# Performance work log

Hardware: AMD Instinct MI355X
Metric: run time of the kernel (lower is better)

## Reference

```python
import jax, jax.numpy as jnp
import numpy as np
from jax import lax

B = 4096          # number of utterance nodes
D_IN = 1856       # 512 audio + 512 visual + 768 text + 64 speaker
H = 128           # hidden_dim
N_STEPS = 4       # fixed-step RK4 steps over t in [0, 1]
ALPHA1, ALPHA2, BETA = 0.8, 0.5, 0.1


def setup_inputs() -> dict:
    key = jax.random.key(0)
    ks = jax.random.split(key, 10)
    features = jax.random.normal(ks[0], (B, D_IN), dtype=jnp.float32)
    speaker_ids = jax.random.randint(ks[1], (B,), 0, 12)
    modality_masks = jax.random.uniform(ks[2], (B, 3), dtype=jnp.float32)
    # params stored as [in, out]; y = x @ W + b (matches torch Linear math)
    s_in = 1.0 / np.sqrt(D_IN)
    Wp = jax.random.uniform(ks[3], (D_IN, H), minval=-s_in, maxval=s_in, dtype=jnp.float32)
    bp = jax.random.uniform(ks[4], (H,), minval=-s_in, maxval=s_in, dtype=jnp.float32)
    s1 = 1.0 / np.sqrt(2 * H)
    W1 = jax.random.uniform(ks[5], (2 * H, H), minval=-s1, maxval=s1, dtype=jnp.float32)
    b1 = jax.random.uniform(ks[6], (H,), minval=-s1, maxval=s1, dtype=jnp.float32)
    s2 = 1.0 / np.sqrt(H)
    W2 = jax.random.uniform(ks[7], (H, H), minval=-s2, maxval=s2, dtype=jnp.float32)
    b2 = jax.random.uniform(ks[8], (H,), minval=-s2, maxval=s2, dtype=jnp.float32)
    return {"features": features, "speaker_ids": speaker_ids,
            "modality_masks": modality_masks, "Wp": Wp, "bp": bp,
            "W1": W1, "b1": b1, "W2": W2, "b2": b2}


def build_graph(speaker_ids, modality_masks):
    idx = jnp.arange(B)
    time_diff = jnp.abs(idx[:, None] - idx[None, :]).astype(jnp.float32)  # [B,B]
    temporal = jnp.exp(-BETA * time_diff)
    same_spk = speaker_ids[:, None] == speaker_ids[None, :]
    # mean_c |m_i,c - m_j,c| without materializing [B,B,3]
    mod_diff = sum(jnp.abs(modality_masks[:, c][:, None] - modality_masks[:, c][None, :])
                   for c in range(3)) * (1.0 / 3.0)
    mod_sim = 1.0 - mod_diff
    off_diag = jnp.where(same_spk, ALPHA1 * temporal, ALPHA2 * temporal * mod_sim)
    adj = jnp.where(idx[:, None] == idx[None, :], 1.0, off_diag)
    adj = adj / (adj.sum(axis=-1, keepdims=True) + 1e-8)
    return adj


def reference(features, speaker_ids, modality_masks, Wp, bp, W1, b1, W2, b2):
    h0 = features @ Wp + bp                      # [B,H] input projection
    adj = build_graph(speaker_ids, modality_masks)

    def ode_func(h):
        h_neighbors = adj @ h                    # [B,H] neighbor aggregation
        h_combined = jnp.concatenate([h, h_neighbors], axis=-1)  # [B,2H]
        return jnp.tanh(h_combined @ W1 + b1) @ W2 + b2

    dt = 1.0 / N_STEPS

    def rk4_step(h, _):
        k1 = ode_func(h)
        k2 = ode_func(h + 0.5 * dt * k1)
        k3 = ode_func(h + 0.5 * dt * k2)
        k4 = ode_func(h + dt * k3)
        return h + (dt / 6.0) * (k1 + 2.0 * k2 + 2.0 * k3 + k4), None

    h_final, _ = lax.scan(rk4_step, h0, None, length=N_STEPS)
    return h_final
```

## Files before the change

kernel.cpp:

```cpp
#include <hip/hip_runtime.h>


typedef unsigned short u16;
typedef unsigned long long u64;
typedef __attribute__((ext_vector_type(8))) short bf16x8v;
typedef __attribute__((ext_vector_type(4))) float f32x4;

#define MFMA16(a, b, c) __builtin_amdgcn_mfma_f32_16x16x32_bf16(a, b, c, 0, 0, 0)

#define BN 4096
#define HN 128
#define DIN 1856
#define TILEW 320

__device__ __forceinline__ float bf2f(u16 u) {
  union { unsigned u; float f; } v; v.u = ((unsigned)u) << 16; return v.f;
}
__device__ __forceinline__ u16 f2bf(float f) {
  union { float f; unsigned u; } v; v.f = f;
  unsigned u = v.u;
  return (u16)((u + 0x7fffu + ((u >> 16) & 1u)) >> 16);
}
__device__ __forceinline__ float ldx(const void* p, long idx, int isf) {
  return isf ? ((const float*)p)[idx] : bf2f(((const u16*)p)[idx]);
}

__device__ __forceinline__ void cstore8(u16* p, u64 v) {
  __hip_atomic_store((u64*)p, v, __ATOMIC_RELAXED, __HIP_MEMORY_SCOPE_AGENT);
}

__global__ __launch_bounds__(256) void detect(
    const void* a0, const void* a1, const void* a2, const void* a3,
    const void* a4, const void* a5, const void* a6, const void* a7,
    const unsigned* spk_raw, int* flags) {
  __shared__ int part[256];
  const int b = blockIdx.x, t = threadIdx.x;
  int cnt = 0;
  if (b < 8) {
    const void* arr[8] = {a0, a1, a2, a3, a4, a5, a6, a7};
    const int nel[8] = {BN * DIN, BN * 3, DIN * HN, HN, 2 * HN * HN, HN, HN * HN, HN};
    const u16* p = (const u16*)arr[b];
    int ns = nel[b] / 2; if (ns > 512) ns = 512;
    for (int e = t; e < ns; e += 256) {
      unsigned ex = (p[2 * e] >> 7) & 0xFFu;
      if (ex < 64u) cnt++;
    }
  } else {
    for (int e = t; e < 512; e += 256)
      if (spk_raw[2 * e + 1] != 0u) cnt++;
  }
  part[t] = cnt;
  __syncthreads();
  #pragma unroll
  for (int o = 128; o > 0; o >>= 1) {
    if (t < o) part[t] += part[t + o];
    __syncthreads();
  }
  if (t == 0) {
    if (b < 8) flags[b] = (part[0] >= 2) ? 1 : 0;
    else       flags[9] = (part[0] == 0) ? 1 : 0;
  }
}

#define FEATBLK 3712
__global__ __launch_bounds__(256) void prep(
    const void* feat, const void* Wp, const void* W1, const void* W2,
    const void* masks, const void* spk, const int* __restrict__ flags,
    u16* featc, u16* WpT, u16* W1T, u16* W2T, float* masks_c, int* spk_c) {
  const int blk = blockIdx.x, t = threadIdx.x;
  if (blk < FEATBLK) {
    long e = ((long)blk * 256 + t) * 8;
    if (flags[0]) {
      const float* pf = (const float*)feat + e;
      u16 r[8];
      #pragma unroll
      for (int k = 0; k < 8; k++) r[k] = f2bf(pf[k]);
      *(bf16x8v*)(featc + e) = *(bf16x8v*)r;
    } else {
      *(bf16x8v*)(featc + e) = *(const bf16x8v*)((const u16*)feat + e);
    }
    return;
  }
  long e = (long)(blk - FEATBLK) * 256 + t;
  const int nWp = DIN * HN, nW1 = 2 * HN * HN, nW2 = HN * HN, nM = BN * 3;
  if (e < nWp) {
    int k = e >> 7, o = e & 127;
    WpT[(long)o * DIN + k] = f2bf(ldx(Wp, e, flags[2]));
    return;
  }
  e -= nWp;
  if (e < nW1) { int k = e >> 7, o = e & 127; W1T[(long)o * 256 + k] = f2bf(ldx(W1, e, flags[4])); return; }
  e -= nW1;
  if (e < nW2) { int k = e >> 7, o = e & 127; W2T[(long)o * 128 + k] = f2bf(ldx(W2, e, flags[6])); return; }
  e -= nW2;
  if (e < nM) { masks_c[e] = ldx(masks, e, flags[1]); return; }
  e -= nM;
  if (e < BN) spk_c[e] = flags[9] ? ((const int*)spk)[2 * e] : ((const int*)spk)[e];
}

__global__ __launch_bounds__(256) void prep2(
    const void* x0, const void* x1, const void* x2,
    const int* __restrict__ flags, float* bp_c, float* b1c, float* b2c) {
  __shared__ float mxs[3][64];
  __shared__ int ord[3];
  const void* bs[3] = {x0, x1, x2};
  const int fl[3] = {flags[3], flags[5], flags[7]};
  const int t = threadIdx.x;
  if (t < 192) {
    int a = t / 64, e = t % 64;
    mxs[a][e] = fmaxf(fabsf(ldx(bs[a], e, fl[a])), fabsf(ldx(bs[a], e + 64, fl[a])));
  }
  __syncthreads();
  if (t == 0) {
    float mx[3];
    for (int a = 0; a < 3; a++) {
      float m = 0.f;
      for (int e = 0; e < 64; e++) m = fmaxf(m, mxs[a][e]);
      mx[a] = m;
    }
    int imin = 0, imax = 0;
    for (int k = 1; k < 3; k++) { if (mx[k] < mx[imin]) imin = k; if (mx[k] > mx[imax]) imax = k; }
    int imid = 3 - imin - imax;
    if (imin == imax) { imin = 0; imid = 1; imax = 2; }
    ord[0] = imin; ord[1] = imid; ord[2] = imax;
  }
  __syncthreads();
  if (t < HN) {
    bp_c[t] = ldx(bs[ord[0]], t, fl[ord[0]]);
    b1c[t]  = ldx(bs[ord[1]], t, fl[ord[1]]);
    b2c[t]  = ldx(bs[ord[2]], t, fl[ord[2]]);
  }
}

__device__ __forceinline__ float adj_raw(int i, int j, int si, float m0, float m1, float m2,
                                         const int* __restrict__ spk,
                                         const float* __restrict__ mk) {
  if (i == j) return 1.0f;
  float t = expf(-0.1f * fabsf((float)(i - j)));
  if (spk[j] == si) return 0.8f * t;
  float ms = fabsf(m0 - mk[j * 3]) + fabsf(m1 - mk[j * 3 + 1]) + fabsf(m2 - mk[j * 3 + 2]);
  return 0.5f * t * (1.0f - ms * (1.0f / 3.0f));
}

__global__ __launch_bounds__(256) void build_band(
    const int* __restrict__ spk, const float* __restrict__ mk, u16* __restrict__ band,
    int* __restrict__ syncf) {
  __shared__ float part[256];
  __shared__ float invs;
  const int i = blockIdx.x, t = threadIdx.x;
  if (t == 0 && i < 256) syncf[i] = 0;
  const int si = spk[i];
  const float m0 = mk[i * 3], m1 = mk[i * 3 + 1], m2 = mk[i * 3 + 2];
  float s = 0.f;
  for (int j = t; j < BN; j += 256) s += adj_raw(i, j, si, m0, m1, m2, spk, mk);
  part[t] = s;
  __syncthreads();
  if (t == 0) {
    float tot = 0.f;
    for (int k = 0; k < 256; k++) tot += part[k];
    invs = 1.0f / (tot + 1e-8f);
  }
  __syncthreads();
  const float inv = invs;
  const int jbase = (i & ~15) - 128;
  for (int k = t; k < TILEW; k += 256) {
    int j = jbase + k;
    float v = 0.f;
    if (j >= 0 && j < BN) v = adj_raw(i, j, si, m0, m1, m2, spk, mk) * inv;
    band[(long)i * TILEW + k] = f2bf(v);
  }
}

#define SNAP_ELEMS ((size_t)HN * BN + 8192)

__global__ __launch_bounds__(512, 2) void fused_ode(
    const u16* __restrict__ featc, const u16* __restrict__ WpT,
    const float* __restrict__ bp_c, const u16* __restrict__ band,
    const u16* __restrict__ W1T, const u16* __restrict__ W2T,
    const float* __restrict__ b1c, const float* __restrict__ b2c,
    u16* __restrict__ hsb, float* __restrict__ outp,
    int* __restrict__ syncf) {
  __shared__ u16 hc[16][264];
  __shared__ u16 zt[16][136];

  const int tid = threadIdx.x, w = tid >> 6, lane = tid & 63;
  const int m = lane & 15, q = lane >> 4;
  const int blk = blockIdx.x;
  const int tile = ((blk & 7) << 5) | (blk >> 3);
  const int r0 = tile * 16, jb = r0 - 128;
  const int n0 = w * 16 + m;
  const int i0 = r0 + q * 4;
  const long base = (long)n0 * BN + i0;

  int nbr = tile - 8 + tid;
  nbr = nbr < 0 ? 0 : (nbr > 255 ? 255 : nbr);

  bf16x8v w1r[8], w2r[4], bnd[10];
  {
    const u16* w1row = W1T + (long)n0 * 256;
    #pragma unroll
    for (int kf = 0; kf < 8; kf++) {
      int k = (kf >> 1) * 64 + (kf & 1) * 32 + q * 8;
      w1r[kf] = *(const bf16x8v*)(w1row + k);
    }
    const u16* w2row = W2T + (long)n0 * 128;
    #pragma unroll
    for (int kf = 0; kf < 4; kf++) {
      int k = (kf >> 1) * 64 + (kf & 1) * 32 + q * 8;
      w2r[kf] = *(const bf16x8v*)(w2row + k);
    }
    const u16* bandrow = band + (long)tile * 5120 + m * TILEW;
    #pragma unroll
    for (int kf = 0; kf < 10; kf++) {
      int k = (kf >> 1) * 64 + (kf & 1) * 32 + q * 8;
      bnd[kf] = *(const bf16x8v*)(bandrow + k);
    }
  }
  const float b1v = b1c[n0], b2v = b2c[n0];

  f32x4 hb;
  {
    f32x4 a0 = {0, 0, 0, 0};
    const u16* arow = featc + (long)(r0 + m) * DIN;
    const u16* brow = WpT + (long)n0 * DIN;
    #pragma unroll 4
    for (int kf = 0; kf < 58; kf++) {
      int k = (kf >> 1) * 64 + (kf & 1) * 32 + q * 8;
      bf16x8v a = *(const bf16x8v*)(arow + k);
      bf16x8v b = *(const bf16x8v*)(brow + k);
      a0 = MFMA16(a, b, a0);
    }
    a0 += bp_c[n0];
    hb = a0;
  }
  f32x4 acc = {0, 0, 0, 0};
  {
    u16* snap0 = hsb + 4096;
    ushort4 hsv;
    hsv.x = f2bf(hb[0]); hsv.y = f2bf(hb[1]); hsv.z = f2bf(hb[2]); hsv.w = f2bf(hb[3]);
    union { ushort4 s; u64 q8; } pu; pu.s = hsv;
    cstore8(&snap0[base], pu.q8);
    hc[q * 4 + 0][n0] = hsv.x; hc[q * 4 + 1][n0] = hsv.y;
    hc[q * 4 + 2][n0] = hsv.z; hc[q * 4 + 3][n0] = hsv.w;
  }
  asm volatile("s_waitcnt vmcnt(0)" ::: "memory");
  __syncthreads();
  if (tid == 0)
    __hip_atomic_store(&syncf[tile], 1, __ATOMIC_RELAXED, __HIP_MEMORY_SCOPE_AGENT);

  const float dt6 = 0.25f / 6.0f;

  #pragma unroll 1
  for (int s = 0; s < 16; s++) {
    const int sub = s & 3;

    if (tid < 20) {
      while (__hip_atomic_load(&syncf[nbr], __ATOMIC_RELAXED,
                               __HIP_MEMORY_SCOPE_AGENT) < s + 1)
        __builtin_amdgcn_s_sleep(1);
    }
    __syncthreads();

    f32x4 g0 = {0, 0, 0, 0};
    const u16* hrow = hsb + (size_t)s * SNAP_ELEMS + 4096 + (long)n0 * BN + jb;
    #pragma unroll
    for (int kf = 0; kf < 10; kf++) {
      int k = (kf >> 1) * 64 + (kf & 1) * 32 + q * 8;
      bf16x8v b = *(const bf16x8v*)(hrow + k);
      g0 = MFMA16(bnd[kf], b, g0);
    }
    #pragma unroll
    for (int r = 0; r < 4; r++) hc[q * 4 + r][128 + n0] = f2bf(g0[r]);
    __syncthreads();

    f32x4 z0 = {0, 0, 0, 0};
    #pragma unroll
    for (int kf = 0; kf < 8; kf++) {
      int k = (kf >> 1) * 64 + (kf & 1) * 32 + q * 8;
      bf16x8v a = *(const bf16x8v*)&hc[m][k];
      z0 = MFMA16(a, w1r[kf], z0);
    }
    #pragma unroll
    for (int r = 0; r < 4; r++) zt[q * 4 + r][n0] = f2bf(tanhf(z0[r] + b1v));
    __syncthreads();

    f32x4 k0 = {0, 0, 0, 0};
    #pragma unroll
    for (int kf = 0; kf < 4; kf++) {
      int k = (kf >> 1) * 64 + (kf & 1) * 32 + q * 8;
      bf16x8v a = *(const bf16x8v*)&zt[m][k];
      k0 = MFMA16(a, w2r[kf], k0);
    }
    f32x4 kv = k0;
    kv += b2v;

    f32x4 hn;
    if (sub == 0)      { acc = 1.f * kv;  hn = hb + 0.125f * kv; }
    else if (sub == 1) { acc += 2.f * kv; hn = hb + 0.125f * kv; }
    else if (sub == 2) { acc += 2.f * kv; hn = hb + 0.25f  * kv; }
    else {
      hn = hb + dt6 * (acc + kv);
      hb = hn;
      if (s == 15) {
        #pragma unroll
        for (int r = 0; r < 4; r++) outp[(long)(i0 + r) * HN + n0] = hn[r];
      }
    }

    if (s < 15) {
      u16* snapw = hsb + (size_t)(s + 1) * SNAP_ELEMS + 4096;
      ushort4 hsv;
      hsv.x = f2bf(hn[0]); hsv.y = f2bf(hn[1]); hsv.z = f2bf(hn[2]); hsv.w = f2bf(hn[3]);
      union { ushort4 s4; u64 q8; } pu; pu.s4 = hsv;
      cstore8(&snapw[base], pu.q8);
      hc[q * 4 + 0][n0] = hsv.x; hc[q * 4 + 1][n0] = hsv.y;
      hc[q * 4 + 2][n0] = hsv.z; hc[q * 4 + 3][n0] = hsv.w;
      asm volatile("s_waitcnt vmcnt(0)" ::: "memory");
      __syncthreads();
      if (tid == 0)
        __hip_atomic_store(&syncf[tile], s + 2, __ATOMIC_RELAXED, __HIP_MEMORY_SCOPE_AGENT);
    }
  }
}

extern "C" void kernel_launch(void* const* d_in, const int* in_sizes, int n_in,
                              void* d_out, int out_size, void* d_ws, size_t ws_size,
                              hipStream_t stream) {
  const void* feat = nullptr; const void* spk = nullptr; const void* masks = nullptr;
  const void* Wp = nullptr; const void* W1 = nullptr; const void* W2 = nullptr;
  const void* bias[3] = {nullptr, nullptr, nullptr};
  int nb = 0;
  for (int k = 0; k < n_in; k++) {
    switch (in_sizes[k]) {
      case BN * DIN:    feat = d_in[k]; break;
      case BN:          spk = d_in[k]; break;
      case BN * 3:      masks = d_in[k]; break;
      case DIN * HN:    Wp = d_in[k]; break;
      case 2 * HN * HN: W1 = d_in[k]; break;
      case HN * HN:     W2 = d_in[k]; break;
      default:          if (in_sizes[k] == HN && nb < 3) bias[nb++] = d_in[k]; break;
    }
  }
  float* out = (float*)d_out;

  char* p = (char*)d_ws;
  int*   flags   = (int*)p;   p += 64;
  int*   spk_c   = (int*)p;   p += BN * 4;
  float* masks_c = (float*)p; p += BN * 3 * 4;
  float* bp_c    = (float*)p; p += 512;
  float* b1c     = (float*)p; p += 512;
  float* b2c     = (float*)p; p += 512;
  int*   syncf   = (int*)p;   p += 1024;
  u16*   featc   = (u16*)p;   p += (size_t)BN * DIN * 2;
  u16*   WpT     = (u16*)p;   p += (size_t)HN * DIN * 2;
  u16*   W1T     = (u16*)p;   p += (size_t)HN * 256 * 2;
  u16*   W2T     = (u16*)p;   p += (size_t)HN * HN * 2;
  u16*   band    = (u16*)p;   p += (size_t)BN * TILEW * 2;
  u16*   hsb     = (u16*)p;   p += 16 * SNAP_ELEMS * 2;
  (void)ws_size; (void)out_size;

  detect<<<9, 256, 0, stream>>>(feat, masks, Wp, bias[0], W1, bias[1], W2, bias[2],
                                (const unsigned*)spk, flags);
  prep<<<FEATBLK + 1184, 256, 0, stream>>>(feat, Wp, W1, W2, masks, spk, flags,
                                           featc, WpT, W1T, W2T, masks_c, spk_c);
  prep2<<<1, 256, 0, stream>>>(bias[0], bias[1], bias[2], flags, bp_c, b1c, b2c);
  build_band<<<BN, 256, 0, stream>>>(spk_c, masks_c, band, syncf);

  fused_ode<<<dim3(BN / 16), dim3(512), 0, stream>>>(
      featc, WpT, bp_c, band, W1T, W2T, b1c, b2c, hsb, out, syncf);
}
```

Before: 248.7 us.

## Fuse band build into ODE kernel, merge prep launches, overlap wait with W1 half

Removes the separate build_band and prep2 kernels. Each ODE block now computes its own 16 adjacency row sums and band coefficients in registers after publishing its initial state, and the bias-ordering work moves into an extra block of prep. Feature conversion is skipped when the input is already bf16, with the ODE reading the raw buffer directly. In the step loop, the first half of the W1 MFMAs (on h, which is already local) is issued before the per-wave neighbor spin-wait, and the block barrier there is replaced by per-wave polling. The costs are redundant adjacency sums inside the persistent kernel, plus a risk of inter-wave LDS hazards now that the barrier is gone.

```diff
diff --git a/kernel.cpp b/kernel.cpp
--- a/kernel.cpp
+++ b/kernel.cpp
@@ -32,7 +32,7 @@
 __global__ __launch_bounds__(256) void detect(
     const void* a0, const void* a1, const void* a2, const void* a3,
     const void* a4, const void* a5, const void* a6, const void* a7,
-    const unsigned* spk_raw, int* flags) {
+    const unsigned* spk_raw, int* flags, int* syncf) {
   __shared__ int part[256];
   const int b = blockIdx.x, t = threadIdx.x;
   int cnt = 0;
@@ -45,9 +45,12 @@
       unsigned ex = (p[2 * e] >> 7) & 0xFFu;
       if (ex < 64u) cnt++;
     }
-  } else {
+  } else if (b == 8) {
     for (int e = t; e < 512; e += 256)
       if (spk_raw[2 * e + 1] != 0u) cnt++;
+  } else {
+    syncf[t] = 0;
+    return;
   }
   part[t] = cnt;
   __syncthreads();
@@ -63,21 +66,53 @@
 }
 
 #define FEATBLK 3712
+#define NWBLK 1184
 __global__ __launch_bounds__(256) void prep(
     const void* feat, const void* Wp, const void* W1, const void* W2,
-    const void* masks, const void* spk, const int* __restrict__ flags,
-    u16* featc, u16* WpT, u16* W1T, u16* W2T, float* masks_c, int* spk_c) {
+    const void* masks, const void* spk,
+    const void* x0, const void* x1, const void* x2,
+    const int* __restrict__ flags,
+    u16* featc, u16* WpT, u16* W1T, u16* W2T, float* masks_c, int* spk_c,
+    float* bp_c, float* b1c, float* b2c) {
+  __shared__ float mxs[3][64];
+  __shared__ int ord[3];
   const int blk = blockIdx.x, t = threadIdx.x;
   if (blk < FEATBLK) {
+    if (!flags[0]) return;
     long e = ((long)blk * 256 + t) * 8;
-    if (flags[0]) {
-      const float* pf = (const float*)feat + e;
-      u16 r[8];
-      #pragma unroll
-      for (int k = 0; k < 8; k++) r[k] = f2bf(pf[k]);
-      *(bf16x8v*)(featc + e) = *(bf16x8v*)r;
-    } else {
-      *(bf16x8v*)(featc + e) = *(const bf16x8v*)((const u16*)feat + e);
+    const float* pf = (const float*)feat + e;
+    u16 r[8];
+    #pragma unroll
+    for (int k = 0; k < 8; k++) r[k] = f2bf(pf[k]);
+    *(bf16x8v*)(featc + e) = *(bf16x8v*)r;
+    return;
+  }
+  if (blk == FEATBLK + NWBLK) {
+    const void* bs[3] = {x0, x1, x2};
+    const int fl[3] = {flags[3], flags[5], flags[7]};
+    if (t < 192) {
+      int a = t / 64, e = t % 64;
+      mxs[a][e] = fmaxf(fabsf(ldx(bs[a], e, fl[a])), fabsf(ldx(bs[a], e + 64, fl[a])));
+    }
+    __syncthreads();
+    if (t == 0) {
+      float mx[3];
+      for (int a = 0; a < 3; a++) {
+        float m = 0.f;
+        for (int e = 0; e < 64; e++) m = fmaxf(m, mxs[a][e]);
+        mx[a] = m;
+      }
+      int imin = 0, imax = 0;
+      for (int k = 1; k < 3; k++) { if (mx[k] < mx[imin]) imin = k; if (mx[k] > mx[imax]) imax = k; }
+      int imid = 3 - imin - imax;
+      if (imin == imax) { imin = 0; imid = 1; imax = 2; }
+      ord[0] = imin; ord[1] = imid; ord[2] = imax;
+    }
+    __syncthreads();
+    if (t < HN) {
+      bp_c[t] = ldx(bs[ord[0]], t, fl[ord[0]]);
+      b1c[t]  = ldx(bs[ord[1]], t, fl[ord[1]]);
+      b2c[t]  = ldx(bs[ord[2]], t, fl[ord[2]]);
     }
     return;
   }
@@ -98,40 +133,6 @@
   if (e < BN) spk_c[e] = flags[9] ? ((const int*)spk)[2 * e] : ((const int*)spk)[e];
 }
 
-__global__ __launch_bounds__(256) void prep2(
-    const void* x0, const void* x1, const void* x2,
-    const int* __restrict__ flags, float* bp_c, float* b1c, float* b2c) {
-  __shared__ float mxs[3][64];
-  __shared__ int ord[3];
-  const void* bs[3] = {x0, x1, x2};
-  const int fl[3] = {flags[3], flags[5], flags[7]};
-  const int t = threadIdx.x;
-  if (t < 192) {
-    int a = t / 64, e = t % 64;
-    mxs[a][e] = fmaxf(fabsf(ldx(bs[a], e, fl[a])), fabsf(ldx(bs[a], e + 64, fl[a])));
-  }
-  __syncthreads();
-  if (t == 0) {
-    float mx[3];
-    for (int a = 0; a < 3; a++) {
-      float m = 0.f;
-      for (int e = 0; e < 64; e++) m = fmaxf(m, mxs[a][e]);
-      mx[a] = m;
-    }
-    int imin = 0, imax = 0;
-    for (int k = 1; k < 3; k++) { if (mx[k] < mx[imin]) imin = k; if (mx[k] > mx[imax]) imax = k; }
-    int imid = 3 - imin - imax;
-    if (imin == imax) { imin = 0; imid = 1; imax = 2; }
-    ord[0] = imin; ord[1] = imid; ord[2] = imax;
-  }
-  __syncthreads();
-  if (t < HN) {
-    bp_c[t] = ldx(bs[ord[0]], t, fl[ord[0]]);
-    b1c[t]  = ldx(bs[ord[1]], t, fl[ord[1]]);
-    b2c[t]  = ldx(bs[ord[2]], t, fl[ord[2]]);
-  }
-}
-
 __device__ __forceinline__ float adj_raw(int i, int j, int si, float m0, float m1, float m2,
                                          const int* __restrict__ spk,
                                          const float* __restrict__ mk) {
@@ -142,46 +143,21 @@
   return 0.5f * t * (1.0f - ms * (1.0f / 3.0f));
 }
 
-__global__ __launch_bounds__(256) void build_band(
-    const int* __restrict__ spk, const float* __restrict__ mk, u16* __restrict__ band,
-    int* __restrict__ syncf) {
-  __shared__ float part[256];
-  __shared__ float invs;
-  const int i = blockIdx.x, t = threadIdx.x;
-  if (t == 0 && i < 256) syncf[i] = 0;
-  const int si = spk[i];
-  const float m0 = mk[i * 3], m1 = mk[i * 3 + 1], m2 = mk[i * 3 + 2];
-  float s = 0.f;
-  for (int j = t; j < BN; j += 256) s += adj_raw(i, j, si, m0, m1, m2, spk, mk);
-  part[t] = s;
-  __syncthreads();
-  if (t == 0) {
-    float tot = 0.f;
-    for (int k = 0; k < 256; k++) tot += part[k];
-    invs = 1.0f / (tot + 1e-8f);
-  }
-  __syncthreads();
-  const float inv = invs;
-  const int jbase = (i & ~15) - 128;
-  for (int k = t; k < TILEW; k += 256) {
-    int j = jbase + k;
-    float v = 0.f;
-    if (j >= 0 && j < BN) v = adj_raw(i, j, si, m0, m1, m2, spk, mk) * inv;
-    band[(long)i * TILEW + k] = f2bf(v);
-  }
-}
-
 #define SNAP_ELEMS ((size_t)HN * BN + 8192)
 
 __global__ __launch_bounds__(512, 2) void fused_ode(
+    const void* __restrict__ feat, const int* __restrict__ flags,
     const u16* __restrict__ featc, const u16* __restrict__ WpT,
-    const float* __restrict__ bp_c, const u16* __restrict__ band,
+    const float* __restrict__ bp_c,
+    const int* __restrict__ spk, const float* __restrict__ mk,
     const u16* __restrict__ W1T, const u16* __restrict__ W2T,
     const float* __restrict__ b1c, const float* __restrict__ b2c,
     u16* __restrict__ hsb, float* __restrict__ outp,
     int* __restrict__ syncf) {
   __shared__ u16 hc[16][264];
   __shared__ u16 zt[16][136];
+  __shared__ float part[16][257];
+  __shared__ float invs[16];
 
   const int tid = threadIdx.x, w = tid >> 6, lane = tid & 63;
   const int m = lane & 15, q = lane >> 4;
@@ -192,7 +168,7 @@
   const int i0 = r0 + q * 4;
   const long base = (long)n0 * BN + i0;
 
-  int nbr = tile - 8 + tid;
+  int nbr = tile - 8 + lane;
   nbr = nbr < 0 ? 0 : (nbr > 255 ? 255 : nbr);
 
   bf16x8v w1r[8], w2r[4], bnd[10];
@@ -209,19 +185,14 @@
       int k = (kf >> 1) * 64 + (kf & 1) * 32 + q * 8;
       w2r[kf] = *(const bf16x8v*)(w2row + k);
     }
-    const u16* bandrow = band + (long)tile * 5120 + m * TILEW;
-    #pragma unroll
-    for (int kf = 0; kf < 10; kf++) {
-      int k = (kf >> 1) * 64 + (kf & 1) * 32 + q * 8;
-      bnd[kf] = *(const bf16x8v*)(bandrow + k);
-    }
   }
   const float b1v = b1c[n0], b2v = b2c[n0];
 
   f32x4 hb;
   {
+    const u16* fbase = flags[0] ? featc : (const u16*)feat;
     f32x4 a0 = {0, 0, 0, 0};
-    const u16* arow = featc + (long)(r0 + m) * DIN;
+    const u16* arow = fbase + (long)(r0 + m) * DIN;
     const u16* brow = WpT + (long)n0 * DIN;
     #pragma unroll 4
     for (int kf = 0; kf < 58; kf++) {
@@ -248,18 +219,65 @@
   if (tid == 0)
     __hip_atomic_store(&syncf[tile], 1, __ATOMIC_RELAXED, __HIP_MEMORY_SCOPE_AGENT);
 
+  {
+    const int tp = tid & 255, rhalf = tid >> 8;
+    #pragma unroll 1
+    for (int p8 = 0; p8 < 8; p8++) {
+      const int r = rhalf + 2 * p8;
+      const int i = r0 + r;
+      const int si = spk[i];
+      const float m0 = mk[i * 3], m1 = mk[i * 3 + 1], m2 = mk[i * 3 + 2];
+      float ssum = 0.f;
+      for (int jj = 0; jj < 16; jj++)
+        ssum += adj_raw(i, tp + (jj << 8), si, m0, m1, m2, spk, mk);
+      part[r][tp] = ssum;
+    }
+  }
+  __syncthreads();
+  if (tid < 16) {
+    float tot = 0.f;
+    for (int k = 0; k < 256; k++) tot += part[tid][k];
+    invs[tid] = 1.0f / (tot + 1e-8f);
+  }
+  __syncthreads();
+  {
+    const int i = r0 + m;
+    const int si = spk[i];
+    const float m0 = mk[i * 3], m1 = mk[i * 3 + 1], m2 = mk[i * 3 + 2];
+    const float inv = invs[m];
+    #pragma unroll
+    for (int kf = 0; kf < 10; kf++) {
+      int k = (kf >> 1) * 64 + (kf & 1) * 32 + q * 8;
+      #pragma unroll
+      for (int e = 0; e < 8; e++) {
+        int j = jb + k + e;
+        float v = 0.f;
+        if (j >= 0 && j < BN) v = adj_raw(i, j, si, m0, m1, m2, spk, mk) * inv;
+        bnd[kf][e] = (short)f2bf(v);
+      }
+    }
+  }
+
   const float dt6 = 0.25f / 6.0f;
 
   #pragma unroll 1
   for (int s = 0; s < 16; s++) {
     const int sub = s & 3;
 
-    if (tid < 20) {
+    f32x4 z0 = {0, 0, 0, 0};
+    #pragma unroll
+    for (int kf = 0; kf < 4; kf++) {
+      int k = (kf >> 1) * 64 + (kf & 1) * 32 + q * 8;
+      bf16x8v a = *(const bf16x8v*)&hc[m][k];
+      z0 = MFMA16(a, w1r[kf], z0);
+    }
+
+    if (lane < 20) {
       while (__hip_atomic_load(&syncf[nbr], __ATOMIC_RELAXED,
                                __HIP_MEMORY_SCOPE_AGENT) < s + 1)
         __builtin_amdgcn_s_sleep(1);
     }
-    __syncthreads();
+    asm volatile("" ::: "memory");
 
     f32x4 g0 = {0, 0, 0, 0};
     const u16* hrow = hsb + (size_t)s * SNAP_ELEMS + 4096 + (long)n0 * BN + jb;
@@ -273,9 +291,8 @@
     for (int r = 0; r < 4; r++) hc[q * 4 + r][128 + n0] = f2bf(g0[r]);
     __syncthreads();
 
-    f32x4 z0 = {0, 0, 0, 0};
-    #pragma unroll
-    for (int kf = 0; kf < 8; kf++) {
+    #pragma unroll
+    for (int kf = 4; kf < 8; kf++) {
       int k = (kf >> 1) * 64 + (kf & 1) * 32 + q * 8;
       bf16x8v a = *(const bf16x8v*)&hc[m][k];
       z0 = MFMA16(a, w1r[kf], z0);
@@ -355,17 +372,16 @@
   u16*   WpT     = (u16*)p;   p += (size_t)HN * DIN * 2;
   u16*   W1T     = (u16*)p;   p += (size_t)HN * 256 * 2;
   u16*   W2T     = (u16*)p;   p += (size_t)HN * HN * 2;
-  u16*   band    = (u16*)p;   p += (size_t)BN * TILEW * 2;
   u16*   hsb     = (u16*)p;   p += 16 * SNAP_ELEMS * 2;
   (void)ws_size; (void)out_size;
 
-  detect<<<9, 256, 0, stream>>>(feat, masks, Wp, bias[0], W1, bias[1], W2, bias[2],
-                                (const unsigned*)spk, flags);
-  prep<<<FEATBLK + 1184, 256, 0, stream>>>(feat, Wp, W1, W2, masks, spk, flags,
-                                           featc, WpT, W1T, W2T, masks_c, spk_c);
-  prep2<<<1, 256, 0, stream>>>(bias[0], bias[1], bias[2], flags, bp_c, b1c, b2c);
-  build_band<<<BN, 256, 0, stream>>>(spk_c, masks_c, band, syncf);
+  detect<<<10, 256, 0, stream>>>(feat, masks, Wp, bias[0], W1, bias[1], W2, bias[2],
+                                 (const unsigned*)spk, flags, syncf);
+  prep<<<FEATBLK + NWBLK + 1, 256, 0, stream>>>(
+      feat, Wp, W1, W2, masks, spk, bias[0], bias[1], bias[2], flags,
+      featc, WpT, W1T, W2T, masks_c, spk_c, bp_c, b1c, b2c);
 
   fused_ode<<<dim3(BN / 16), dim3(512), 0, stream>>>(
-      featc, WpT, bp_c, band, W1T, W2T, b1c, b2c, hsb, out, syncf);
-}
+      feat, flags, featc, WpT, bp_c, spk_c, masks_c, W1T, W2T, b1c, b2c,
+      hsb, out, syncf);
+}
```

New measurement: 296.0 us. 1.19x slower.

## Merge prep kernels, skip bf16 feature copy, overlap W1 half with neighbor wait

Applied to the files above, without the earlier changes.

Folds prep2 and build_band into the prep kernel and moves syncf zeroing into detect, cutting the launch sequence from five kernels to three. The band builder now reads raw speaker ids and masks directly instead of staging them in converted workspace copies. When features are already bf16, the copy into featc is skipped and fused_ode reads the input pointer directly. Inside the ODE loop, the first half of the W1 product, which uses only the local h, is computed before the spin-wait on neighbor tiles so it overlaps the wait.

```diff
diff --git a/kernel.cpp b/kernel.cpp
--- a/kernel.cpp
+++ b/kernel.cpp
@@ -24,6 +24,9 @@
 __device__ __forceinline__ float ldx(const void* p, long idx, int isf) {
   return isf ? ((const float*)p)[idx] : bf2f(((const u16*)p)[idx]);
 }
+__device__ __forceinline__ int ldspk(const void* spk, int j, int i64) {
+  return i64 ? ((const int*)spk)[2 * j] : ((const int*)spk)[j];
+}
 
 __device__ __forceinline__ void cstore8(u16* p, u64 v) {
   __hip_atomic_store((u64*)p, v, __ATOMIC_RELAXED, __HIP_MEMORY_SCOPE_AGENT);
@@ -32,7 +35,7 @@
 __global__ __launch_bounds__(256) void detect(
     const void* a0, const void* a1, const void* a2, const void* a3,
     const void* a4, const void* a5, const void* a6, const void* a7,
-    const unsigned* spk_raw, int* flags) {
+    const unsigned* spk_raw, int* flags, int* syncf) {
   __shared__ int part[256];
   const int b = blockIdx.x, t = threadIdx.x;
   int cnt = 0;
@@ -45,9 +48,12 @@
       unsigned ex = (p[2 * e] >> 7) & 0xFFu;
       if (ex < 64u) cnt++;
     }
-  } else {
+  } else if (b == 8) {
     for (int e = t; e < 512; e += 256)
       if (spk_raw[2 * e + 1] != 0u) cnt++;
+  } else {
+    syncf[t] = 0;
+    return;
   }
   part[t] = cnt;
   __syncthreads();
@@ -62,118 +68,117 @@
   }
 }
 
+__device__ __forceinline__ float adjr(int i, int j, int si, float m0, float m1, float m2,
+                                      const void* __restrict__ spk,
+                                      const void* __restrict__ mk, int fm, int fs) {
+  if (i == j) return 1.0f;
+  float t = expf(-0.1f * fabsf((float)(i - j)));
+  if (ldspk(spk, j, fs) == si) return 0.8f * t;
+  float ms = fabsf(m0 - ldx(mk, (long)j * 3, fm)) +
+             fabsf(m1 - ldx(mk, (long)j * 3 + 1, fm)) +
+             fabsf(m2 - ldx(mk, (long)j * 3 + 2, fm));
+  return 0.5f * t * (1.0f - ms * (1.0f / 3.0f));
+}
+
 #define FEATBLK 3712
+#define NWBLK 1120
 __global__ __launch_bounds__(256) void prep(
     const void* feat, const void* Wp, const void* W1, const void* W2,
-    const void* masks, const void* spk, const int* __restrict__ flags,
-    u16* featc, u16* WpT, u16* W1T, u16* W2T, float* masks_c, int* spk_c) {
+    const void* masks, const void* spk,
+    const void* x0, const void* x1, const void* x2,
+    const int* __restrict__ flags,
+    u16* featc, u16* WpT, u16* W1T, u16* W2T,
+    float* bp_c, float* b1c, float* b2c, u16* __restrict__ band) {
+  __shared__ float part[256];
+  __shared__ float invs;
+  __shared__ float mxs[3][64];
+  __shared__ int ord[3];
   const int blk = blockIdx.x, t = threadIdx.x;
   if (blk < FEATBLK) {
+    if (!flags[0]) return;
     long e = ((long)blk * 256 + t) * 8;
-    if (flags[0]) {
-      const float* pf = (const float*)feat + e;
-      u16 r[8];
-      #pragma unroll
-      for (int k = 0; k < 8; k++) r[k] = f2bf(pf[k]);
-      *(bf16x8v*)(featc + e) = *(bf16x8v*)r;
-    } else {
-      *(bf16x8v*)(featc + e) = *(const bf16x8v*)((const u16*)feat + e);
-    }
+    const float* pf = (const float*)feat + e;
+    u16 r[8];
+    #pragma unroll
+    for (int k = 0; k < 8; k++) r[k] = f2bf(pf[k]);
+    *(bf16x8v*)(featc + e) = *(bf16x8v*)r;
     return;
   }
-  long e = (long)(blk - FEATBLK) * 256 + t;
-  const int nWp = DIN * HN, nW1 = 2 * HN * HN, nW2 = HN * HN, nM = BN * 3;
-  if (e < nWp) {
-    int k = e >> 7, o = e & 127;
-    WpT[(long)o * DIN + k] = f2bf(ldx(Wp, e, flags[2]));
+  if (blk < FEATBLK + NWBLK) {
+    long e = (long)(blk - FEATBLK) * 256 + t;
+    const int nWp = DIN * HN, nW1 = 2 * HN * HN;
+    if (e < nWp) {
+      int k = e >> 7, o = e & 127;
+      WpT[(long)o * DIN + k] = f2bf(ldx(Wp, e, flags[2]));
+      return;
+    }
+    e -= nWp;
+    if (e < nW1) { int k = e >> 7, o = e & 127; W1T[(long)o * 256 + k] = f2bf(ldx(W1, e, flags[4])); return; }
+    e -= nW1;
+    { int k = e >> 7, o = e & 127; W2T[(long)o * 128 + k] = f2bf(ldx(W2, e, flags[6])); }
     return;
   }
-  e -= nWp;
-  if (e < nW1) { int k = e >> 7, o = e & 127; W1T[(long)o * 256 + k] = f2bf(ldx(W1, e, flags[4])); return; }
-  e -= nW1;
-  if (e < nW2) { int k = e >> 7, o = e & 127; W2T[(long)o * 128 + k] = f2bf(ldx(W2, e, flags[6])); return; }
-  e -= nW2;
-  if (e < nM) { masks_c[e] = ldx(masks, e, flags[1]); return; }
-  e -= nM;
-  if (e < BN) spk_c[e] = flags[9] ? ((const int*)spk)[2 * e] : ((const int*)spk)[e];
-}
-
-__global__ __launch_bounds__(256) void prep2(
-    const void* x0, const void* x1, const void* x2,
-    const int* __restrict__ flags, float* bp_c, float* b1c, float* b2c) {
-  __shared__ float mxs[3][64];
-  __shared__ int ord[3];
-  const void* bs[3] = {x0, x1, x2};
-  const int fl[3] = {flags[3], flags[5], flags[7]};
-  const int t = threadIdx.x;
-  if (t < 192) {
-    int a = t / 64, e = t % 64;
-    mxs[a][e] = fmaxf(fabsf(ldx(bs[a], e, fl[a])), fabsf(ldx(bs[a], e + 64, fl[a])));
-  }
-  __syncthreads();
-  if (t == 0) {
-    float mx[3];
-    for (int a = 0; a < 3; a++) {
-      float m = 0.f;
-      for (int e = 0; e < 64; e++) m = fmaxf(m, mxs[a][e]);
-      mx[a] = m;
-    }
-    int imin = 0, imax = 0;
-    for (int k = 1; k < 3; k++) { if (mx[k] < mx[imin]) imin = k; if (mx[k] > mx[imax]) imax = k; }
-    int imid = 3 - imin - imax;
-    if (imin == imax) { imin = 0; imid = 1; imax = 2; }
-    ord[0] = imin; ord[1] = imid; ord[2] = imax;
-  }
-  __syncthreads();
-  if (t < HN) {
-    bp_c[t] = ldx(bs[ord[0]], t, fl[ord[0]]);
-    b1c[t]  = ldx(bs[ord[1]], t, fl[ord[1]]);
-    b2c[t]  = ldx(bs[ord[2]], t, fl[ord[2]]);
-  }
-}
-
-__device__ __forceinline__ float adj_raw(int i, int j, int si, float m0, float m1, float m2,
-                                         const int* __restrict__ spk,
-                                         const float* __restrict__ mk) {
-  if (i == j) return 1.0f;
-  float t = expf(-0.1f * fabsf((float)(i - j)));
-  if (spk[j] == si) return 0.8f * t;
-  float ms = fabsf(m0 - mk[j * 3]) + fabsf(m1 - mk[j * 3 + 1]) + fabsf(m2 - mk[j * 3 + 2]);
-  return 0.5f * t * (1.0f - ms * (1.0f / 3.0f));
-}
-
-__global__ __launch_bounds__(256) void build_band(
-    const int* __restrict__ spk, const float* __restrict__ mk, u16* __restrict__ band,
-    int* __restrict__ syncf) {
-  __shared__ float part[256];
-  __shared__ float invs;
-  const int i = blockIdx.x, t = threadIdx.x;
-  if (t == 0 && i < 256) syncf[i] = 0;
-  const int si = spk[i];
-  const float m0 = mk[i * 3], m1 = mk[i * 3 + 1], m2 = mk[i * 3 + 2];
-  float s = 0.f;
-  for (int j = t; j < BN; j += 256) s += adj_raw(i, j, si, m0, m1, m2, spk, mk);
-  part[t] = s;
-  __syncthreads();
-  if (t == 0) {
-    float tot = 0.f;
-    for (int k = 0; k < 256; k++) tot += part[k];
-    invs = 1.0f / (tot + 1e-8f);
-  }
-  __syncthreads();
-  const float inv = invs;
-  const int jbase = (i & ~15) - 128;
-  for (int k = t; k < TILEW; k += 256) {
-    int j = jbase + k;
-    float v = 0.f;
-    if (j >= 0 && j < BN) v = adj_raw(i, j, si, m0, m1, m2, spk, mk) * inv;
-    band[(long)i * TILEW + k] = f2bf(v);
+  if (blk == FEATBLK + NWBLK) {
+    const void* bs[3] = {x0, x1, x2};
+    const int fl[3] = {flags[3], flags[5], flags[7]};
+    if (t < 192) {
+      int a = t / 64, e = t % 64;
+      mxs[a][e] = fmaxf(fabsf(ldx(bs[a], e, fl[a])), fabsf(ldx(bs[a], e + 64, fl[a])));
+    }
+    __syncthreads();
+    if (t == 0) {
+      float mx[3];
+      for (int a = 0; a < 3; a++) {
+        float m = 0.f;
+        for (int e = 0; e < 64; e++) m = fmaxf(m, mxs[a][e]);
+        mx[a] = m;
+      }
+      int imin = 0, imax = 0;
+      for (int k = 1; k < 3; k++) { if (mx[k] < mx[imin]) imin = k; if (mx[k] > mx[imax]) imax = k; }
+      int imid = 3 - imin - imax;
+      if (imin == imax) { imin = 0; imid = 1; imax = 2; }
+      ord[0] = imin; ord[1] = imid; ord[2] = imax;
+    }
+    __syncthreads();
+    if (t < HN) {
+      bp_c[t] = ldx(bs[ord[0]], t, fl[ord[0]]);
+      b1c[t]  = ldx(bs[ord[1]], t, fl[ord[1]]);
+      b2c[t]  = ldx(bs[ord[2]], t, fl[ord[2]]);
+    }
+    return;
+  }
+  {
+    const int i = blk - FEATBLK - NWBLK - 1;
+    const int fm = flags[1], fs = flags[9];
+    const int si = ldspk(spk, i, fs);
+    const float m0 = ldx(masks, (long)i * 3, fm);
+    const float m1 = ldx(masks, (long)i * 3 + 1, fm);
+    const float m2 = ldx(masks, (long)i * 3 + 2, fm);
+    float s = 0.f;
+    for (int j = t; j < BN; j += 256) s += adjr(i, j, si, m0, m1, m2, spk, masks, fm, fs);
+    part[t] = s;
+    __syncthreads();
+    if (t == 0) {
+      float tot = 0.f;
+      for (int k = 0; k < 256; k++) tot += part[k];
+      invs = 1.0f / (tot + 1e-8f);
+    }
+    __syncthreads();
+    const float inv = invs;
+    const int jbase = (i & ~15) - 128;
+    for (int k = t; k < TILEW; k += 256) {
+      int j = jbase + k;
+      float v = 0.f;
+      if (j >= 0 && j < BN) v = adjr(i, j, si, m0, m1, m2, spk, masks, fm, fs) * inv;
+      band[(long)i * TILEW + k] = f2bf(v);
+    }
   }
 }
 
 #define SNAP_ELEMS ((size_t)HN * BN + 8192)
 
 __global__ __launch_bounds__(512, 2) void fused_ode(
+    const void* __restrict__ feat, const int* __restrict__ flags,
     const u16* __restrict__ featc, const u16* __restrict__ WpT,
     const float* __restrict__ bp_c, const u16* __restrict__ band,
     const u16* __restrict__ W1T, const u16* __restrict__ W2T,
@@ -220,8 +225,9 @@
 
   f32x4 hb;
   {
+    const u16* fbase = flags[0] ? featc : (const u16*)feat;
     f32x4 a0 = {0, 0, 0, 0};
-    const u16* arow = featc + (long)(r0 + m) * DIN;
+    const u16* arow = fbase + (long)(r0 + m) * DIN;
     const u16* brow = WpT + (long)n0 * DIN;
     #pragma unroll 4
     for (int kf = 0; kf < 58; kf++) {
@@ -254,6 +260,14 @@
   for (int s = 0; s < 16; s++) {
     const int sub = s & 3;
 
+    f32x4 z0 = {0, 0, 0, 0};
+    #pragma unroll
+    for (int kf = 0; kf < 4; kf++) {
+      int k = (kf >> 1) * 64 + (kf & 1) * 32 + q * 8;
+      bf16x8v a = *(const bf16x8v*)&hc[m][k];
+      z0 = MFMA16(a, w1r[kf], z0);
+    }
+
     if (tid < 20) {
       while (__hip_atomic_load(&syncf[nbr], __ATOMIC_RELAXED,
                                __HIP_MEMORY_SCOPE_AGENT) < s + 1)
@@ -273,9 +287,8 @@
     for (int r = 0; r < 4; r++) hc[q * 4 + r][128 + n0] = f2bf(g0[r]);
     __syncthreads();
 
-    f32x4 z0 = {0, 0, 0, 0};
-    #pragma unroll
-    for (int kf = 0; kf < 8; kf++) {
+    #pragma unroll
+    for (int kf = 4; kf < 8; kf++) {
       int k = (kf >> 1) * 64 + (kf & 1) * 32 + q * 8;
       bf16x8v a = *(const bf16x8v*)&hc[m][k];
       z0 = MFMA16(a, w1r[kf], z0);
@@ -345,8 +358,6 @@
 
   char* p = (char*)d_ws;
   int*   flags   = (int*)p;   p += 64;
-  int*   spk_c   = (int*)p;   p += BN * 4;
-  float* masks_c = (float*)p; p += BN * 3 * 4;
   float* bp_c    = (float*)p; p += 512;
   float* b1c     = (float*)p; p += 512;
   float* b2c     = (float*)p; p += 512;
@@ -359,13 +370,13 @@
   u16*   hsb     = (u16*)p;   p += 16 * SNAP_ELEMS * 2;
   (void)ws_size; (void)out_size;
 
-  detect<<<9, 256, 0, stream>>>(feat, masks, Wp, bias[0], W1, bias[1], W2, bias[2],
-                                (const unsigned*)spk, flags);
-  prep<<<FEATBLK + 1184, 256, 0, stream>>>(feat, Wp, W1, W2, masks, spk, flags,
-                                           featc, WpT, W1T, W2T, masks_c, spk_c);
-  prep2<<<1, 256, 0, stream>>>(bias[0], bias[1], bias[2], flags, bp_c, b1c, b2c);
-  build_band<<<BN, 256, 0, stream>>>(spk_c, masks_c, band, syncf);
+  detect<<<10, 256, 0, stream>>>(feat, masks, Wp, bias[0], W1, bias[1], W2, bias[2],
+                                 (const unsigned*)spk, flags, syncf);
+  prep<<<FEATBLK + NWBLK + 1 + BN, 256, 0, stream>>>(
+      feat, Wp, W1, W2, masks, spk, bias[0], bias[1], bias[2], flags,
+      featc, WpT, W1T, W2T, bp_c, b1c, b2c, band);
 
   fused_ode<<<dim3(BN / 16), dim3(512), 0, stream>>>(
-      featc, WpT, bp_c, band, W1T, W2T, b1c, b2c, hsb, out, syncf);
-}
+      feat, flags, featc, WpT, bp_c, band, W1T, W2T, b1c, b2c,
+      hsb, out, syncf);
+}
```

After: 251.5 us. Within noise of the previous version (+1.1%).
